# Kernel optimization log

Hardware: AMD Instinct MI355X
Metric: run time of the kernel (lower is better)

The kernel has to match this reference:

```python
import jax, jax.numpy as jnp
import numpy as np

B, N_FEAT, EMB, ATT = 8192, 32, 30, 10


def setup_inputs() -> dict:
    key = jax.random.key(0)
    k1, k2, k3, k4 = jax.random.split(key, 4)
    x = jax.random.normal(k1, (B, N_FEAT, EMB), dtype=jnp.float32)
    attention_w = jax.random.normal(k2, (EMB, ATT), dtype=jnp.float32) * 0.05
    attention_b = jax.random.normal(k3, (ATT,), dtype=jnp.float32) * 0.05
    attention_h = jax.random.normal(k4, (ATT,), dtype=jnp.float32) * 0.05
    attention_p = jnp.ones((EMB, 1), dtype=jnp.float32)
    return {"x": x, "attention_w": attention_w, "attention_b": attention_b,
            "attention_h": attention_h, "attention_p": attention_p}


def reference(x, attention_w, attention_b, attention_h, attention_p):
    # x: [B, n, E] -> pairwise element-wise products over upper-triangular (i<j) pairs
    n = x.shape[1]
    idx_i, idx_j = np.triu_indices(n, k=1)  # static index lists, P = n(n-1)/2
    prod = x[:, idx_i, :] * x[:, idx_j, :]  # [B, P, E]
    # attention MLP: relu(prod @ W + b), score = <relu, h>
    wx = jnp.einsum('bpe,ea->bpa', prod, attention_w) + attention_b  # [B, P, A]
    score = jnp.sum(jax.nn.relu(wx) * attention_h, axis=2, keepdims=True)  # [B, P, 1]
    # softmax over interactions (exp / sum-exp in original, same math)
    att = jax.nn.softmax(score, axis=1)  # [B, P, 1]
    afm = jnp.sum(att * prod, axis=1)  # [B, E]
    return afm @ attention_p  # [B, 1]
```

## Files before the change

### kernel.cpp

```cpp
#include <hip/hip_runtime.h>
#include <math.h>

#define NFEAT 32
#define EMB   30
#define ATT   10
#define NPAIR 496
#define BLK   128
#define WPB   2
#define ROWSTR 36

typedef float v2f __attribute__((ext_vector_type(2)));

#define PK_FMA_BCLO(acc, pr, w) \
    asm("v_pk_fma_f32 %0, %1, %2, %0 op_sel:[0,0,0] op_sel_hi:[0,1,1]" \
        : "+v"(acc) : "v"(pr), "s"(w))
#define PK_FMA_BCHI(acc, pr, w) \
    asm("v_pk_fma_f32 %0, %1, %2, %0 op_sel:[1,0,0] op_sel_hi:[1,1,1]" \
        : "+v"(acc) : "v"(pr), "s"(w))
#define PK_FMA(acc, a, b) \
    asm("v_pk_fma_f32 %0, %1, %2, %0" : "+v"(acc) : "v"(a), "s"(b))
#define PK_MUL(d, a, b) \
    asm("v_pk_mul_f32 %0, %1, %2" : "=v"(d) : "v"(a), "v"(b))

__global__ __launch_bounds__(BLK) __attribute__((amdgpu_waves_per_eu(3)))
void attn_net_kernel(const float* __restrict__ x,
                     const float* __restrict__ W,
                     const float* __restrict__ bias,
                     const float* __restrict__ h,
                     const float* __restrict__ pvec,
                     float* __restrict__ out)
{
    __shared__ __align__(16) float sx[WPB * NFEAT * ROWSTR];

    const int t    = threadIdx.x;
    const int wid  = t >> 6;
    const int lane = t & 63;
    const int b    = blockIdx.x * WPB + wid;

    float* swx = sx + wid * (NFEAT * ROWSTR);
    {
        const float4* xin = reinterpret_cast<const float4*>(x + (size_t)b * (NFEAT * EMB));
        for (int v = lane; v < 240; v += 64) {
            const float4 d = xin[v];
            const int ef = 4 * v;
            #pragma unroll
            for (int u = 0; u < 4; ++u) {
                const int e = ef + u;
                const int r = e / EMB;
                const int c = e - r * EMB;
                swx[r * ROWSTR + c] = ((const float*)&d)[u];
            }
        }
    }

    v2f b2[5], h2[5];
    #pragma unroll
    for (int a2 = 0; a2 < 5; ++a2) {
        b2[a2] = v2f{bias[2 * a2], bias[2 * a2 + 1]};
        h2[a2] = v2f{h[2 * a2],    h[2 * a2 + 1]};
    }

    float m = -INFINITY, se = 0.f, sec = 0.f;

    #pragma unroll
    for (int ch = 0; ch < 2; ++ch) {
        const int T = ch * 64 + lane;
        const bool special = (T >= 120);
        int r0, r1, c0, c1;
        if (special) {
            const int s7 = T - 120;
            r0 = 4 * s7; r1 = r0 + 2; c0 = r0 + 1; c1 = r0 + 3;
        } else {
            const float sq = sqrtf((float)(961 - 8 * T));
            const int I = (int)((31.0f - sq) * 0.5f);
            const int J = I + 1 + (T - ((I * (31 - I)) >> 1));
            r0 = 2 * I; r1 = r0 + 1; c0 = 2 * J; c1 = c0 + 1;
        }
        const int oi0 = r0 * ROWSTR, oi1 = r1 * ROWSTR;
        const int oj0 = c0 * ROWSTR, oj1 = c1 * ROWSTR;

        v2f acc[4][5];
        v2f accC[4];
        #pragma unroll
        for (int p = 0; p < 4; ++p) {
            #pragma unroll
            for (int a2 = 0; a2 < 5; ++a2) acc[p][a2] = b2[a2];
            accC[p] = v2f{0.f, 0.f};
        }

        #pragma unroll
        for (int eg = 0; eg < 8; ++eg) {
            const int e0 = eg * 4;
            const bool full = (eg < 7);
            v2f wa[5], wb[5], wc[5], wd[5];
            #pragma unroll
            for (int a2 = 0; a2 < 5; ++a2) {
                wa[a2] = v2f{W[(e0    ) * ATT + 2*a2], W[(e0    ) * ATT + 2*a2 + 1]};
                wb[a2] = v2f{W[(e0 + 1) * ATT + 2*a2], W[(e0 + 1) * ATT + 2*a2 + 1]};
            }
            if (full) {
                #pragma unroll
                for (int a2 = 0; a2 < 5; ++a2) {
                    wc[a2] = v2f{W[(e0 + 2) * ATT + 2*a2], W[(e0 + 2) * ATT + 2*a2 + 1]};
                    wd[a2] = v2f{W[(e0 + 3) * ATT + 2*a2], W[(e0 + 3) * ATT + 2*a2 + 1]};
                }
            }
            const v2f pv01 = v2f{pvec[e0], pvec[e0 + 1]};
            v2f pv23 = v2f{0.f, 0.f};
            if (full) pv23 = v2f{pvec[e0 + 2], pvec[e0 + 3]};

            const float4 xi0 = *reinterpret_cast<const float4*>(&swx[oi0 + e0]);
            const float4 xi1 = *reinterpret_cast<const float4*>(&swx[oi1 + e0]);

            auto do_pair = [&](v2f* ap, v2f& cp, const float4& xi, const float4& xj) {
                const v2f* xiv = reinterpret_cast<const v2f*>(&xi);
                const v2f* xjv = reinterpret_cast<const v2f*>(&xj);
                v2f prL;
                PK_MUL(prL, xiv[0], xjv[0]);
                #pragma unroll
                for (int a2 = 0; a2 < 5; ++a2) PK_FMA_BCLO(ap[a2], prL, wa[a2]);
                #pragma unroll
                for (int a2 = 0; a2 < 5; ++a2) PK_FMA_BCHI(ap[a2], prL, wb[a2]);
                PK_FMA(cp, prL, pv01);
                if (full) {
                    v2f prH;
                    PK_MUL(prH, xiv[1], xjv[1]);
                    #pragma unroll
                    for (int a2 = 0; a2 < 5; ++a2) PK_FMA_BCLO(ap[a2], prH, wc[a2]);
                    #pragma unroll
                    for (int a2 = 0; a2 < 5; ++a2) PK_FMA_BCHI(ap[a2], prH, wd[a2]);
                    PK_FMA(cp, prH, pv23);
                }
            };

            {
                const float4 xj = *reinterpret_cast<const float4*>(&swx[oj0 + e0]);
                do_pair(acc[0], accC[0], xi0, xj);
                do_pair(acc[2], accC[2], xi1, xj);
            }
            {
                const float4 xj = *reinterpret_cast<const float4*>(&swx[oj1 + e0]);
                do_pair(acc[1], accC[1], xi0, xj);
                do_pair(acc[3], accC[3], xi1, xj);
            }
        }

        float s4[4], cv4[4];
        #pragma unroll
        for (int p = 0; p < 4; ++p) {
            const v2f z = v2f{0.f, 0.f};
            v2f sv = z;
            #pragma unroll
            for (int a2 = 0; a2 < 5; ++a2) {
                const v2f r = __builtin_elementwise_max(acc[p][a2], z);
                sv = __builtin_elementwise_fma(r, h2[a2], sv);
            }
            s4[p]  = sv.x + sv.y;
            cv4[p] = accC[p].x + accC[p].y;
        }
        if (special) { s4[1] = -INFINITY; s4[2] = -INFINITY; }

        const float nm = fmaxf(m, fmaxf(fmaxf(s4[0], s4[1]), fmaxf(s4[2], s4[3])));
        const float scale = __expf(m - nm);
        se  *= scale;
        sec *= scale;
        #pragma unroll
        for (int p = 0; p < 4; ++p) {
            const float E = __expf(s4[p] - nm);
            se += E;
            sec = fmaf(E, cv4[p], sec);
        }
        m = nm;
    }

    float M = m;
    #pragma unroll
    for (int o = 1; o < 64; o <<= 1) M = fmaxf(M, __shfl_xor(M, o, 64));
    const float rs = __expf(m - M);
    se  *= rs;
    sec *= rs;
    #pragma unroll
    for (int o = 1; o < 64; o <<= 1) {
        se  += __shfl_xor(se,  o, 64);
        sec += __shfl_xor(sec, o, 64);
    }
    if (lane == 0) out[b] = sec / se;
}

extern "C" void kernel_launch(void* const* d_in, const int* in_sizes, int n_in,
                              void* d_out, int out_size, void* d_ws, size_t ws_size,
                              hipStream_t stream) {
    const float* x    = (const float*)d_in[0];
    const float* W    = (const float*)d_in[1];
    const float* bias = (const float*)d_in[2];
    const float* h    = (const float*)d_in[3];
    const float* pvec = (const float*)d_in[4];
    float* out = (float*)d_out;

    const int B = in_sizes[0] / (NFEAT * EMB);
    attn_net_kernel<<<B / WPB, BLK, 0, stream>>>(x, W, bias, h, pvec, out);
}
```

Measured before the change: 37.71 us.

## Split each batch row across two wavefronts with shared-memory softmax merge

```diff
diff --git a/kernel.cpp b/kernel.cpp
--- a/kernel.cpp
+++ b/kernel.cpp
@@ -6,7 +6,6 @@
 #define ATT   10
 #define NPAIR 496
 #define BLK   128
-#define WPB   2
 #define ROWSTR 36
 
 typedef float v2f __attribute__((ext_vector_type(2)));
@@ -30,17 +29,17 @@
                      const float* __restrict__ pvec,
                      float* __restrict__ out)
 {
-    __shared__ __align__(16) float sx[WPB * NFEAT * ROWSTR];
+    __shared__ __align__(16) float sx[NFEAT * ROWSTR];
+    __shared__ float red[2][3];
 
     const int t    = threadIdx.x;
     const int wid  = t >> 6;
     const int lane = t & 63;
-    const int b    = blockIdx.x * WPB + wid;
-
-    float* swx = sx + wid * (NFEAT * ROWSTR);
+    const int b    = blockIdx.x;
+
     {
         const float4* xin = reinterpret_cast<const float4*>(x + (size_t)b * (NFEAT * EMB));
-        for (int v = lane; v < 240; v += 64) {
+        for (int v = t; v < 240; v += BLK) {
             const float4 d = xin[v];
             const int ef = 4 * v;
             #pragma unroll
@@ -48,7 +47,7 @@
                 const int e = ef + u;
                 const int r = e / EMB;
                 const int c = e - r * EMB;
-                swx[r * ROWSTR + c] = ((const float*)&d)[u];
+                sx[r * ROWSTR + c] = ((const float*)&d)[u];
             }
         }
     }
@@ -60,131 +59,135 @@
         h2[a2] = v2f{h[2 * a2],    h[2 * a2 + 1]};
     }
 
-    float m = -INFINITY, se = 0.f, sec = 0.f;
-
-    #pragma unroll
-    for (int ch = 0; ch < 2; ++ch) {
-        const int T = ch * 64 + lane;
-        const bool special = (T >= 120);
-        int r0, r1, c0, c1;
-        if (special) {
-            const int s7 = T - 120;
-            r0 = 4 * s7; r1 = r0 + 2; c0 = r0 + 1; c1 = r0 + 3;
-        } else {
-            const float sq = sqrtf((float)(961 - 8 * T));
-            const int I = (int)((31.0f - sq) * 0.5f);
-            const int J = I + 1 + (T - ((I * (31 - I)) >> 1));
-            r0 = 2 * I; r1 = r0 + 1; c0 = 2 * J; c1 = c0 + 1;
-        }
-        const int oi0 = r0 * ROWSTR, oi1 = r1 * ROWSTR;
-        const int oj0 = c0 * ROWSTR, oj1 = c1 * ROWSTR;
-
-        v2f acc[4][5];
-        v2f accC[4];
+    __syncthreads();
+
+    const int T = wid * 64 + lane;
+    const bool special = (T >= 120);
+    int r0, r1, c0, c1;
+    if (special) {
+        const int s7 = T - 120;
+        r0 = 4 * s7; r1 = r0 + 2; c0 = r0 + 1; c1 = r0 + 3;
+    } else {
+        const float sq = sqrtf((float)(961 - 8 * T));
+        const int I = (int)((31.0f - sq) * 0.5f);
+        const int J = I + 1 + (T - ((I * (31 - I)) >> 1));
+        r0 = 2 * I; r1 = r0 + 1; c0 = 2 * J; c1 = c0 + 1;
+    }
+    const int oi0 = r0 * ROWSTR, oi1 = r1 * ROWSTR;
+    const int oj0 = c0 * ROWSTR, oj1 = c1 * ROWSTR;
+
+    v2f acc[4][5];
+    v2f accC[4];
+    #pragma unroll
+    for (int p = 0; p < 4; ++p) {
         #pragma unroll
-        for (int p = 0; p < 4; ++p) {
-            #pragma unroll
-            for (int a2 = 0; a2 < 5; ++a2) acc[p][a2] = b2[a2];
-            accC[p] = v2f{0.f, 0.f};
-        }
-
+        for (int a2 = 0; a2 < 5; ++a2) acc[p][a2] = b2[a2];
+        accC[p] = v2f{0.f, 0.f};
+    }
+
+    #pragma unroll
+    for (int eg = 0; eg < 8; ++eg) {
+        const int e0 = eg * 4;
+        const bool full = (eg < 7);
+        v2f wa[5], wb[5], wc[5], wd[5];
         #pragma unroll
-        for (int eg = 0; eg < 8; ++eg) {
-            const int e0 = eg * 4;
-            const bool full = (eg < 7);
-            v2f wa[5], wb[5], wc[5], wd[5];
+        for (int a2 = 0; a2 < 5; ++a2) {
+            wa[a2] = v2f{W[(e0    ) * ATT + 2*a2], W[(e0    ) * ATT + 2*a2 + 1]};
+            wb[a2] = v2f{W[(e0 + 1) * ATT + 2*a2], W[(e0 + 1) * ATT + 2*a2 + 1]};
+        }
+        if (full) {
             #pragma unroll
             for (int a2 = 0; a2 < 5; ++a2) {
-                wa[a2] = v2f{W[(e0    ) * ATT + 2*a2], W[(e0    ) * ATT + 2*a2 + 1]};
-                wb[a2] = v2f{W[(e0 + 1) * ATT + 2*a2], W[(e0 + 1) * ATT + 2*a2 + 1]};
+                wc[a2] = v2f{W[(e0 + 2) * ATT + 2*a2], W[(e0 + 2) * ATT + 2*a2 + 1]};
+                wd[a2] = v2f{W[(e0 + 3) * ATT + 2*a2], W[(e0 + 3) * ATT + 2*a2 + 1]};
             }
+        }
+        const v2f pv01 = v2f{pvec[e0], pvec[e0 + 1]};
+        v2f pv23 = v2f{0.f, 0.f};
+        if (full) pv23 = v2f{pvec[e0 + 2], pvec[e0 + 3]};
+
+        const float4 xi0 = *reinterpret_cast<const float4*>(&sx[oi0 + e0]);
+        const float4 xi1 = *reinterpret_cast<const float4*>(&sx[oi1 + e0]);
+
+        auto do_pair = [&](v2f* ap, v2f& cp, const float4& xi, const float4& xj) {
+            const v2f* xiv = reinterpret_cast<const v2f*>(&xi);
+            const v2f* xjv = reinterpret_cast<const v2f*>(&xj);
+            v2f prL;
+            PK_MUL(prL, xiv[0], xjv[0]);
+            #pragma unroll
+            for (int a2 = 0; a2 < 5; ++a2) PK_FMA_BCLO(ap[a2], prL, wa[a2]);
+            #pragma unroll
+            for (int a2 = 0; a2 < 5; ++a2) PK_FMA_BCHI(ap[a2], prL, wb[a2]);
+            PK_FMA(cp, prL, pv01);
             if (full) {
+                v2f prH;
+                PK_MUL(prH, xiv[1], xjv[1]);
                 #pragma unroll
-                for (int a2 = 0; a2 < 5; ++a2) {
-                    wc[a2] = v2f{W[(e0 + 2) * ATT + 2*a2], W[(e0 + 2) * ATT + 2*a2 + 1]};
-                    wd[a2] = v2f{W[(e0 + 3) * ATT + 2*a2], W[(e0 + 3) * ATT + 2*a2 + 1]};
-                }
+                for (int a2 = 0; a2 < 5; ++a2) PK_FMA_BCLO(ap[a2], prH, wc[a2]);
+                #pragma unroll
+                for (int a2 = 0; a2 < 5; ++a2) PK_FMA_BCHI(ap[a2], prH, wd[a2]);
+                PK_FMA(cp, prH, pv23);
             }
-            const v2f pv01 = v2f{pvec[e0], pvec[e0 + 1]};
-            v2f pv23 = v2f{0.f, 0.f};
-            if (full) pv23 = v2f{pvec[e0 + 2], pvec[e0 + 3]};
-
-            const float4 xi0 = *reinterpret_cast<const float4*>(&swx[oi0 + e0]);
-            const float4 xi1 = *reinterpret_cast<const float4*>(&swx[oi1 + e0]);
-
-            auto do_pair = [&](v2f* ap, v2f& cp, const float4& xi, const float4& xj) {
-                const v2f* xiv = reinterpret_cast<const v2f*>(&xi);
-                const v2f* xjv = reinterpret_cast<const v2f*>(&xj);
-                v2f prL;
-                PK_MUL(prL, xiv[0], xjv[0]);
-                #pragma unroll
-                for (int a2 = 0; a2 < 5; ++a2) PK_FMA_BCLO(ap[a2], prL, wa[a2]);
-                #pragma unroll
-                for (int a2 = 0; a2 < 5; ++a2) PK_FMA_BCHI(ap[a2], prL, wb[a2]);
-                PK_FMA(cp, prL, pv01);
-                if (full) {
-                    v2f prH;
-                    PK_MUL(prH, xiv[1], xjv[1]);
-                    #pragma unroll
-                    for (int a2 = 0; a2 < 5; ++a2) PK_FMA_BCLO(ap[a2], prH, wc[a2]);
-                    #pragma unroll
-                    for (int a2 = 0; a2 < 5; ++a2) PK_FMA_BCHI(ap[a2], prH, wd[a2]);
-                    PK_FMA(cp, prH, pv23);
-                }
-            };
-
-            {
-                const float4 xj = *reinterpret_cast<const float4*>(&swx[oj0 + e0]);
-                do_pair(acc[0], accC[0], xi0, xj);
-                do_pair(acc[2], accC[2], xi1, xj);
-            }
-            {
-                const float4 xj = *reinterpret_cast<const float4*>(&swx[oj1 + e0]);
-                do_pair(acc[1], accC[1], xi0, xj);
-                do_pair(acc[3], accC[3], xi1, xj);
-            }
-        }
-
-        float s4[4], cv4[4];
+        };
+
+        {
+            const float4 xj = *reinterpret_cast<const float4*>(&sx[oj0 + e0]);
+            do_pair(acc[0], accC[0], xi0, xj);
+            do_pair(acc[2], accC[2], xi1, xj);
+        }
+        {
+            const float4 xj = *reinterpret_cast<const float4*>(&sx[oj1 + e0]);
+            do_pair(acc[1], accC[1], xi0, xj);
+            do_pair(acc[3], accC[3], xi1, xj);
+        }
+    }
+
+    float s4[4], cv4[4];
+    #pragma unroll
+    for (int p = 0; p < 4; ++p) {
+        const v2f z = v2f{0.f, 0.f};
+        v2f sv = z;
         #pragma unroll
-        for (int p = 0; p < 4; ++p) {
-            const v2f z = v2f{0.f, 0.f};
-            v2f sv = z;
-            #pragma unroll
-            for (int a2 = 0; a2 < 5; ++a2) {
-                const v2f r = __builtin_elementwise_max(acc[p][a2], z);
-                sv = __builtin_elementwise_fma(r, h2[a2], sv);
-            }
-            s4[p]  = sv.x + sv.y;
-            cv4[p] = accC[p].x + accC[p].y;
-        }
-        if (special) { s4[1] = -INFINITY; s4[2] = -INFINITY; }
-
-        const float nm = fmaxf(m, fmaxf(fmaxf(s4[0], s4[1]), fmaxf(s4[2], s4[3])));
-        const float scale = __expf(m - nm);
-        se  *= scale;
-        sec *= scale;
-        #pragma unroll
-        for (int p = 0; p < 4; ++p) {
-            const float E = __expf(s4[p] - nm);
-            se += E;
-            sec = fmaf(E, cv4[p], sec);
-        }
+        for (int a2 = 0; a2 < 5; ++a2) {
+            const v2f r = __builtin_elementwise_max(acc[p][a2], z);
+            sv = __builtin_elementwise_fma(r, h2[a2], sv);
+        }
+        s4[p]  = sv.x + sv.y;
+        cv4[p] = accC[p].x + accC[p].y;
+    }
+    if (special) { s4[1] = -INFINITY; s4[2] = -INFINITY; }
+
+    float m = fmaxf(fmaxf(s4[0], s4[1]), fmaxf(s4[2], s4[3]));
+    float se = 0.f, sec = 0.f;
+    #pragma unroll
+    for (int p = 0; p < 4; ++p) {
+        const float E = __expf(s4[p] - m);
+        se += E;
+        sec = fmaf(E, cv4[p], sec);
+    }
+
+    #pragma unroll
+    for (int o = 1; o < 64; o <<= 1) {
+        const float om  = __shfl_xor(m,   o, 64);
+        const float ose = __shfl_xor(se,  o, 64);
+        const float osc = __shfl_xor(sec, o, 64);
+        const float nm  = fmaxf(m, om);
+        const float ea  = __expf(m  - nm);
+        const float eb  = __expf(om - nm);
+        se  = fmaf(se,  ea, ose * eb);
+        sec = fmaf(sec, ea, osc * eb);
         m = nm;
     }
-
-    float M = m;
-    #pragma unroll
-    for (int o = 1; o < 64; o <<= 1) M = fmaxf(M, __shfl_xor(M, o, 64));
-    const float rs = __expf(m - M);
-    se  *= rs;
-    sec *= rs;
-    #pragma unroll
-    for (int o = 1; o < 64; o <<= 1) {
-        se  += __shfl_xor(se,  o, 64);
-        sec += __shfl_xor(sec, o, 64);
-    }
-    if (lane == 0) out[b] = sec / se;
+    if (lane == 0) { red[wid][0] = m; red[wid][1] = se; red[wid][2] = sec; }
+    __syncthreads();
+    if (t == 0) {
+        const float m0 = red[0][0], m1 = red[1][0];
+        const float M  = fmaxf(m0, m1);
+        const float e0 = __expf(m0 - M), e1 = __expf(m1 - M);
+        const float SE  = red[0][1] * e0 + red[1][1] * e1;
+        const float SEC = red[0][2] * e0 + red[1][2] * e1;
+        out[b] = SEC / SE;
+    }
 }
 
 extern "C" void kernel_launch(void* const* d_in, const int* in_sizes, int n_in,
@@ -198,5 +201,5 @@
     float* out = (float*)d_out;
 
     const int B = in_sizes[0] / (NFEAT * EMB);
-    attn_net_kernel<<<B / WPB, BLK, 0, stream>>>(x, W, bias, h, pvec, out);
+    attn_net_kernel<<<B, BLK, 0, stream>>>(x, W, bias, h, pvec, out);
 }
```

Result: slower. 41.00 us (+8.7%).
